# Kernel optimization log

Hardware: AMD Instinct MI355X
Metric: run time of the kernel (lower is better)

The kernel has to match this reference:

```python
import jax, jax.numpy as jnp
import numpy as np

B, NDET, NT, NY, NX = 4, 128, 2048, 256, 256
D, L, NH, PS = 256, 6, 8, 16
HP, WP = NY // PS, NX // PS
N = HP * WP


def setup_inputs() -> dict:
    key = jax.random.key(0)
    ks = jax.random.split(key, 12)
    w = lambda k, s: jax.random.normal(k, s, jnp.float32) * 0.02
    sino = jax.random.normal(ks[0], (B, 1, NDET, NT), jnp.float32)
    # LUT: channel 0 = floor temporal index (float, some out-of-range -> masked), channel 1 = interp alpha
    kf = jax.random.randint(ks[1], (NY, NX, NDET), -8, NT).astype(jnp.float32)
    alpha = jax.random.uniform(ks[2], (NY, NX, NDET), dtype=jnp.float32)
    lut = jnp.stack([kf, alpha], axis=-1)
    return {
        "sino": sino, "lut": lut,
        "patch_w": w(ks[3], (D, PS * PS)), "patch_b": jnp.zeros((D,), jnp.float32),
        "pos_embed": w(ks[4], (1, N, D)),
        "ln1_g": jnp.ones((L, D), jnp.float32), "ln1_b": jnp.zeros((L, D), jnp.float32),
        "wqkv": w(ks[5], (L, 3 * D, D)), "bqkv": jnp.zeros((L, 3 * D), jnp.float32),
        "wo": w(ks[6], (L, D, D)), "bo": jnp.zeros((L, D), jnp.float32),
        "ln2_g": jnp.ones((L, D), jnp.float32), "ln2_b": jnp.zeros((L, D), jnp.float32),
        "w1": w(ks[7], (L, 4 * D, D)), "b1": jnp.zeros((L, 4 * D), jnp.float32),
        "w2": w(ks[8], (L, D, 4 * D)), "b2": jnp.zeros((L, D), jnp.float32),
        "proj_w": w(ks[9], (PS * PS, D)), "proj_b": jnp.zeros((PS * PS,), jnp.float32),
        "conv_w": w(ks[10], (1, 1, 3, 3)), "conv_b": jnp.zeros((1,), jnp.float32),
    }


def _layernorm(x, g, b):
    m = x.mean(-1, keepdims=True)
    v = x.var(-1, keepdims=True)
    return (x - m) / jnp.sqrt(v + 1e-5) * g + b


def _mha(x, wqkv, bqkv, wo, bo):
    Bq, Nt, Dd = x.shape
    hd = Dd // NH
    qkv = x @ wqkv.T + bqkv                       # [B,N,3D]
    q, k, v = jnp.split(qkv, 3, axis=-1)
    sp = lambda t: t.reshape(Bq, Nt, NH, hd).transpose(0, 2, 1, 3)  # [B,H,N,hd]
    q, k, v = sp(q), sp(k), sp(v)
    scores = jnp.einsum('bhnd,bhmd->bhnm', q, k) / jnp.sqrt(jnp.float32(hd))
    att = jax.nn.softmax(scores, axis=-1)
    o = jnp.einsum('bhnm,bhmd->bhnd', att, v).transpose(0, 2, 1, 3).reshape(Bq, Nt, Dd)
    return o @ wo.T + bo


def _backproject(sino, lut):
    # sino: [B,1,n_det,n_t]; lut: [ny,nx,n_det,2] -> image [B,1,ny,nx]
    n_t = sino.shape[-1]
    kf = lut[..., 0].astype(jnp.int32)
    alpha = lut[..., 1]
    valid = (kf >= 0) & (kf < n_t - 1)
    k0 = jnp.clip(kf, 0, n_t - 2)
    k1 = k0 + 1
    S = sino[:, 0]                                # [B, n_det, n_t]
    d_idx = jnp.arange(NDET)[None, None, :]       # broadcast over (ny, nx)

    def per_batch(Sb):                            # Sb: [n_det, n_t]
        s0 = Sb[d_idx, k0]                        # [ny,nx,n_det]
        s1 = Sb[d_idx, k1]
        sk = (1.0 - alpha) * s0 + alpha * s1
        return jnp.where(valid, sk, 0.0)

    sk = jax.vmap(per_batch)(S)                   # [B,ny,nx,n_det]
    apod = 0.5 - 0.5 * jnp.cos(2.0 * jnp.pi * jnp.arange(NDET) / (NDET - 1))
    apod = apod.astype(sino.dtype)
    out = jnp.einsum('byxd,d->byx', sk, apod) / jnp.maximum(apod.sum(), 1e-6)
    return out[:, None]                           # [B,1,ny,nx]


def reference(sino, lut, patch_w, patch_b, pos_embed, ln1_g, ln1_b, wqkv, bqkv,
              wo, bo, ln2_g, ln2_b, w1, b1, w2, b2, proj_w, proj_b, conv_w, conv_b):
    bp_img = _backproject(sino, lut)              # [B,1,NY,NX]
    # patch embed (Conv2d k=stride=patch  ==  patch-flatten + linear)
    x = bp_img[:, 0].reshape(B, HP, PS, WP, PS).transpose(0, 1, 3, 2, 4).reshape(B, N, PS * PS)
    z = x @ patch_w.T + patch_b                   # [B,N,D]
    z = z + pos_embed
    for l in range(L):
        y = _layernorm(z, ln1_g[l], ln1_b[l])
        z = z + _mha(y, wqkv[l], bqkv[l], wo[l], bo[l])
        y = _layernorm(z, ln2_g[l], ln2_b[l])
        y = jax.nn.gelu(y @ w1[l].T + b1[l], approximate=False) @ w2[l].T + b2[l]
        z = z + y
    pixels = z @ proj_w.T + proj_b                # [B,N,PS*PS]
    pixels = pixels.reshape(B, HP, WP, PS, PS).transpose(0, 1, 3, 2, 4)
    img = pixels.reshape(B, 1, HP * PS, WP * PS)
    img = jax.lax.conv_general_dilated(img, conv_w, (1, 1), 'SAME',
                                       dimension_numbers=('NCHW', 'OIHW', 'NCHW'))
    img = img + conv_b.reshape(1, 1, 1, 1)
    img = img + bp_img                            # residual (shapes match)
    return (img, bp_img)
```

## Files before the change

kernel.cpp:

```cpp
#include <hip/hip_runtime.h>
#include <hip/hip_bf16.h>
#include <math.h>

#define BB 4
#define NDET 128
#define NT 2048
#define DD 256
#define LL 6
#define MROWS 1024

typedef __attribute__((ext_vector_type(8))) short s8v;
typedef __attribute__((ext_vector_type(4))) float f32x4;
typedef unsigned short ushort_t;

__device__ __forceinline__ unsigned short f2b(float x) {
  union { float f; unsigned u; } v; v.f = x;
  unsigned r = v.u + 0x7fff + ((v.u >> 16) & 1);
  return (unsigned short)(r >> 16);
}
__device__ __forceinline__ unsigned pk2(float a, float b) {
  return (unsigned)f2b(a) | ((unsigned)f2b(b) << 16);
}
__device__ __forceinline__ float gelu_exact(float x) {
  return 0.5f * x * (1.0f + erff(x * 0.70710678118654752f));
}

__global__ __launch_bounds__(256) void cast_all(
    const float* __restrict__ s0, const float* __restrict__ s1,
    const float* __restrict__ s2, const float* __restrict__ s3,
    const float* __restrict__ s4, const float* __restrict__ s5,
    unsigned short* __restrict__ d0, unsigned short* __restrict__ d1,
    unsigned short* __restrict__ d2, unsigned short* __restrict__ d3,
    unsigned short* __restrict__ d4, unsigned short* __restrict__ d5,
    const float* __restrict__ sino, float* __restrict__ st)
{
  const int e0 = 16384, e1 = 311296, e2 = 409600, e3 = 802816, e4 = 1196032,
            e5 = 1212416, e6 = 1474560;
  int i = blockIdx.x * 256 + threadIdx.x;
  int stride = gridDim.x * 256;
  for (; i < e6; i += stride) {
    if (i < e5) {
      const float* s; unsigned short* d; int j;
      if (i < e0)      { s = s0; d = d0; j = i; }
      else if (i < e1) { s = s1; d = d1; j = i - e0; }
      else if (i < e2) { s = s2; d = d2; j = i - e1; }
      else if (i < e3) { s = s3; d = d3; j = i - e2; }
      else if (i < e4) { s = s4; d = d4; j = i - e3; }
      else             { s = s5; d = d5; j = i - e4; }
      float4 f = ((const float4*)s)[j];
      uint2 uv;
      uv.x = pk2(f.x, f.y);
      uv.y = pk2(f.z, f.w);
      ((uint2*)d)[j] = uv;
    } else {
      int idx = i - e5;
      float4 v;
      v.x = sino[idx];
      v.y = sino[262144 + idx];
      v.z = sino[524288 + idx];
      v.w = sino[786432 + idx];
      ((float4*)st)[idx] = v;
    }
  }
}

__global__ __launch_bounds__(256) void bp_part(
    const float* __restrict__ st, const float* __restrict__ lut,
    float* __restrict__ partial)
{
  __shared__ float apod[NDET];
  int tid = threadIdx.x;
  if (tid < NDET) {
    float ap = 0.5f - 0.5f * cosf(6.283185307179586f * (float)tid / 127.0f);
    apod[tid] = ap * (1.0f / 63.5f);
  }
  __syncthreads();
  int c = blockIdx.x & 7;
  int pb = blockIdx.x >> 3;
  int pix = pb * 256 + tid;
  const float* lrow = lut + (size_t)pix * 256;
  const float4* sp = (const float4*)st;
  float a0 = 0.f, a1 = 0.f, a2 = 0.f, a3 = 0.f;
#pragma unroll
  for (int d0 = c * 16; d0 < c * 16 + 16; d0 += 4) {
    float4 l0 = *(const float4*)(lrow + d0 * 2);
    float4 l1 = *(const float4*)(lrow + d0 * 2 + 4);
    float kfs[4] = {l0.x, l0.z, l1.x, l1.z};
    float als[4] = {l0.y, l0.w, l1.y, l1.w};
#pragma unroll
    for (int dd = 0; dd < 4; ++dd) {
      int kf = (int)kfs[dd];
      if (kf >= 0 && kf < NT - 1) {
        float al = als[dd];
        float ap = apod[d0 + dd];
        float w0 = (1.0f - al) * ap, w1 = al * ap;
        const float4* q = sp + (d0 + dd) * NT + kf;
        float4 s0 = q[0], s1 = q[1];
        a0 += w0 * s0.x + w1 * s1.x;
        a1 += w0 * s0.y + w1 * s1.y;
        a2 += w0 * s0.z + w1 * s1.z;
        a3 += w0 * s0.w + w1 * s1.w;
      }
    }
  }
  partial[(size_t)(c * 4 + 0) * 65536 + pix] = a0;
  partial[(size_t)(c * 4 + 1) * 65536 + pix] = a1;
  partial[(size_t)(c * 4 + 2) * 65536 + pix] = a2;
  partial[(size_t)(c * 4 + 3) * 65536 + pix] = a3;
}

__global__ __launch_bounds__(256) void bp_reduce(
    const float* __restrict__ partial, float* __restrict__ bp,
    float* __restrict__ out_bp)
{
  int pix = blockIdx.x * 256 + threadIdx.x;
#pragma unroll
  for (int b = 0; b < 4; ++b) {
    float s = 0.f;
#pragma unroll
    for (int c = 0; c < 8; ++c) s += partial[(size_t)(c * 4 + b) * 65536 + pix];
    bp[b * 65536 + pix] = s;
    out_bp[b * 65536 + pix] = s;
  }
}

template<int ACT, int RES, int AMODE, int OMODE, int TN>
__global__ __launch_bounds__(256) void gemm4(
    const float* __restrict__ A, const unsigned short* __restrict__ A16,
    const unsigned short* __restrict__ Wb,
    const float* __restrict__ bias, const float* __restrict__ res,
    const float* __restrict__ lng, const float* __restrict__ lnb,
    float* __restrict__ C, unsigned short* __restrict__ C16,
    int N, int K, int res_mask)
{
  constexpr int NJ = TN / 32;
  __shared__ __align__(16) unsigned short As[32][264];
  __shared__ __align__(16) unsigned short Bs[TN][264];
  int bm = blockIdx.y * 32, bn = blockIdx.x * TN;
  int tid = threadIdx.x;
  int lane = tid & 63, w = tid >> 6;
  int lr = lane & 15, hi = lane >> 4;
  int lk = hi * 8, lg = hi * 4;
  int wr = (w & 1) * 16, wc = (w >> 1) * (TN / 2 == 32 ? 32 : 16);
  f32x4 acc[NJ];
#pragma unroll
  for (int j = 0; j < NJ; ++j) acc[j] = (f32x4){0.f, 0.f, 0.f, 0.f};

  for (int kc = 0; kc < K; kc += 256) {
    if (kc) __syncthreads();
    if (AMODE == 2) {
      float4 gl = ((const float4*)lng)[lane];
      float4 bl = ((const float4*)lnb)[lane];
#pragma unroll
      for (int rr = 0; rr < 8; ++rr) {
        int row = w * 8 + rr;
        float4 v = ((const float4*)(A + (size_t)(bm + row) * 256))[lane];
        float s = v.x + v.y + v.z + v.w;
#pragma unroll
        for (int off = 32; off; off >>= 1) s += __shfl_xor(s, off);
        float mean = s * (1.0f / 256.0f);
        float q = (v.x - mean) * (v.x - mean) + (v.y - mean) * (v.y - mean) +
                  (v.z - mean) * (v.z - mean) + (v.w - mean) * (v.w - mean);
#pragma unroll
        for (int off = 32; off; off >>= 1) q += __shfl_xor(q, off);
        float inv = 1.0f / sqrtf(q * (1.0f / 256.0f) + 1e-5f);
        float y0 = (v.x - mean) * inv * gl.x + bl.x;
        float y1 = (v.y - mean) * inv * gl.y + bl.y;
        float y2 = (v.z - mean) * inv * gl.z + bl.z;
        float y3 = (v.w - mean) * inv * gl.w + bl.w;
        uint2 u2; u2.x = pk2(y0, y1); u2.y = pk2(y2, y3);
        *(uint2*)&As[row][lane * 4] = u2;
      }
    } else if (AMODE == 3) {
      int r = tid >> 3, cb = (tid & 7) * 32;
      const unsigned short* ap = A16 + (size_t)(bm + r) * K + kc + cb;
#pragma unroll
      for (int q8 = 0; q8 < 4; ++q8)
        *(uint4*)&As[r][cb + q8 * 8] = *(const uint4*)(ap + q8 * 8);
    } else {
      int r = tid >> 3, cb = (tid & 7) * 32;
#pragma unroll
      for (int q8 = 0; q8 < 4; ++q8) {
        int k = cb + q8 * 8;
        float4 f0, f1;
        if (AMODE == 0) {
          const float* ap = A + (size_t)(bm + r) * K + kc + k;
          f0 = *(const float4*)ap;
          f1 = *(const float4*)(ap + 4);
        } else {
          int m = bm + r;
          int bb = m >> 8, nn = m & 255;
          int k2 = k + 4;
          f0 = *(const float4*)(A + (size_t)bb * 65536 +
               ((nn >> 4) * 16 + (k >> 4)) * 256 + (nn & 15) * 16 + (k & 15));
          f1 = *(const float4*)(A + (size_t)bb * 65536 +
               ((nn >> 4) * 16 + (k2 >> 4)) * 256 + (nn & 15) * 16 + (k2 & 15));
        }
        uint4 u;
        u.x = pk2(f0.x, f0.y); u.y = pk2(f0.z, f0.w);
        u.z = pk2(f1.x, f1.y); u.w = pk2(f1.z, f1.w);
        *(uint4*)&As[r][k] = u;
      }
    }
    if (TN == 64) {
      int r = tid >> 2, cb = (tid & 3) * 64;
      const unsigned short* wp = Wb + (size_t)(bn + r) * K + kc + cb;
#pragma unroll
      for (int q8 = 0; q8 < 8; ++q8)
        *(uint4*)&Bs[r][cb + q8 * 8] = *(const uint4*)(wp + q8 * 8);
    } else {
      int r = tid >> 3, cb = (tid & 7) * 32;
      const unsigned short* wp = Wb + (size_t)(bn + r) * K + kc + cb;
#pragma unroll
      for (int q8 = 0; q8 < 4; ++q8)
        *(uint4*)&Bs[r][cb + q8 * 8] = *(const uint4*)(wp + q8 * 8);
    }
    __syncthreads();
#pragma unroll
    for (int k0 = 0; k0 < 256; k0 += 32) {
      s8v a = *(const s8v*)&As[wr + lr][k0 + lk];
      s8v b0 = *(const s8v*)&Bs[wc + lr][k0 + lk];
      acc[0] = __builtin_amdgcn_mfma_f32_16x16x32_bf16(a, b0, acc[0], 0, 0, 0);
      if (NJ == 2) {
        s8v b1 = *(const s8v*)&Bs[wc + 16 + lr][k0 + lk];
        acc[1] = __builtin_amdgcn_mfma_f32_16x16x32_bf16(a, b1, acc[1], 0, 0, 0);
      }
    }
  }

#pragma unroll
  for (int j = 0; j < NJ; ++j) {
    int n = bn + wc + j * 16 + lr;
    float bv = bias[n];
#pragma unroll
    for (int r4 = 0; r4 < 4; ++r4) {
      int m = bm + wr + lg + r4;
      float c = acc[j][r4] + bv;
      if (ACT == 1) c = gelu_exact(c);
      if (RES == 1) c += res[(size_t)(m & res_mask) * N + n];
      if (OMODE == 0) {
        C[(size_t)m * N + n] = c;
      } else if (OMODE == 1) {
        int bb = m >> 8, t2 = m & 255;
        C[(size_t)bb * 65536 + ((t2 >> 4) * 16 + (n >> 4)) * 256 +
          (t2 & 15) * 16 + (n & 15)] = c;
      } else {
        C16[(size_t)m * N + n] = f2b(c);
      }
    }
  }
}

__global__ __launch_bounds__(256) void attn_fused(
    const unsigned short* __restrict__ qkv, unsigned short* __restrict__ o16)
{
  __shared__ __align__(16) unsigned short Kl[256][40];
  __shared__ __align__(16) unsigned short Qb[32][40];
  __shared__ __align__(16) unsigned short Vt[32][264];
  __shared__ __align__(16) char sp[34304];
  float (*Sf)[268] = (float(*)[268])sp;
  unsigned short (*Pl)[264] = (unsigned short(*)[264])sp;
  int bi = blockIdx.x;
  int qc = bi & 7, h = (bi >> 3) & 7, b = bi >> 6;
  int tid = threadIdx.x, lane = tid & 63, w = tid >> 6;
  int lr = lane & 15, hi = lane >> 4;
  int lk = hi * 8, lg = hi * 4;
  const unsigned short* base = qkv + (size_t)b * 256 * 768;

  {
    const unsigned short* kr = base + tid * 768 + 256 + h * 32;
#pragma unroll
    for (int cq = 0; cq < 4; ++cq)
      *(uint4*)&Kl[tid][cq * 8] = *(const uint4*)(kr + cq * 8);
    const unsigned short* vr = base + tid * 768 + 512 + h * 32;
    unsigned short tmp[32];
#pragma unroll
    for (int cq = 0; cq < 4; ++cq)
      *(uint4*)&tmp[cq * 8] = *(const uint4*)(vr + cq * 8);
#pragma unroll
    for (int cc = 0; cc < 32; ++cc) Vt[cc][tid] = tmp[cc];
    int row = tid >> 3, c0 = (tid & 7) * 4;
    *(uint2*)&Qb[row][c0] =
        *(const uint2*)(base + (qc * 32 + row) * 768 + h * 32 + c0);
  }
  __syncthreads();

  {
    s8v qa0 = *(const s8v*)&Qb[lr][lk];
    s8v qa1 = *(const s8v*)&Qb[16 + lr][lk];
    f32x4 z4 = (f32x4){0.f, 0.f, 0.f, 0.f};
#pragma unroll
    for (int j = 0; j < 4; ++j) {
      s8v kb = *(const s8v*)&Kl[w * 64 + j * 16 + lr][lk];
      f32x4 s0 = __builtin_amdgcn_mfma_f32_16x16x32_bf16(qa0, kb, z4, 0, 0, 0);
      f32x4 s1 = __builtin_amdgcn_mfma_f32_16x16x32_bf16(qa1, kb, z4, 0, 0, 0);
#pragma unroll
      for (int r4 = 0; r4 < 4; ++r4) {
        Sf[lg + r4][w * 64 + j * 16 + lr] = s0[r4];
        Sf[16 + lg + r4][w * 64 + j * 16 + lr] = s1[r4];
      }
    }
  }
  __syncthreads();

  float vv[8][4];
  {
    const float scale = 0.17677669529663687f;
#pragma unroll
    for (int rr = 0; rr < 8; ++rr) {
      int row = w * 8 + rr;
      float4 v = *(const float4*)&Sf[row][lane * 4];
      v.x *= scale; v.y *= scale; v.z *= scale; v.w *= scale;
      float mx = fmaxf(fmaxf(v.x, v.y), fmaxf(v.z, v.w));
#pragma unroll
      for (int off = 32; off; off >>= 1) mx = fmaxf(mx, __shfl_xor(mx, off));
      float e0 = expf(v.x - mx), e1 = expf(v.y - mx);
      float e2 = expf(v.z - mx), e3 = expf(v.w - mx);
      float ss = e0 + e1 + e2 + e3;
#pragma unroll
      for (int off = 32; off; off >>= 1) ss += __shfl_xor(ss, off);
      float inv = 1.0f / ss;
      vv[rr][0] = e0 * inv; vv[rr][1] = e1 * inv;
      vv[rr][2] = e2 * inv; vv[rr][3] = e3 * inv;
    }
  }
  __syncthreads();
#pragma unroll
  for (int rr = 0; rr < 8; ++rr) {
    int row = w * 8 + rr;
    uint2 u2;
    u2.x = pk2(vv[rr][0], vv[rr][1]);
    u2.y = pk2(vv[rr][2], vv[rr][3]);
    *(uint2*)&Pl[row][lane * 4] = u2;
  }
  __syncthreads();

  {
    int wr = (w & 1) * 16, wc2 = (w >> 1) * 16;
    f32x4 oa = (f32x4){0.f, 0.f, 0.f, 0.f};
#pragma unroll
    for (int ks = 0; ks < 8; ++ks) {
      s8v pa = *(const s8v*)&Pl[wr + lr][ks * 32 + lk];
      s8v vb = *(const s8v*)&Vt[wc2 + lr][ks * 32 + lk];
      oa = __builtin_amdgcn_mfma_f32_16x16x32_bf16(pa, vb, oa, 0, 0, 0);
    }
#pragma unroll
    for (int r4 = 0; r4 < 4; ++r4) {
      int row = qc * 32 + wr + lg + r4;
      o16[((size_t)(b * 256) + row) * 256 + h * 32 + wc2 + lr] = f2b(oa[r4]);
    }
  }
}

__global__ __launch_bounds__(256) void conv_kernel(
    const float* __restrict__ img, const float* __restrict__ cw,
    const float* __restrict__ cb, const float* __restrict__ bp,
    float* __restrict__ out_img)
{
  int gid = blockIdx.x * 256 + threadIdx.x;
  int b = gid >> 16, rem = gid & 65535;
  int y = rem >> 8, x = rem & 255;
  const float* ip = img + (size_t)b * 65536;
  float s = cb[0];
#pragma unroll
  for (int dy = -1; dy <= 1; ++dy)
#pragma unroll
    for (int dx = -1; dx <= 1; ++dx) {
      int yy = y + dy, xx = x + dx;
      if (yy >= 0 && yy < 256 && xx >= 0 && xx < 256)
        s += cw[(dy + 1) * 3 + (dx + 1)] * ip[yy * 256 + xx];
    }
  out_img[gid] = s + bp[gid];
}

extern "C" void kernel_launch(void* const* d_in, const int* in_sizes, int n_in,
                              void* d_out, int out_size, void* d_ws, size_t ws_size,
                              hipStream_t stream) {
  const float* sino    = (const float*)d_in[0];
  const float* lut     = (const float*)d_in[1];
  const float* patch_w = (const float*)d_in[2];
  const float* patch_b = (const float*)d_in[3];
  const float* pos     = (const float*)d_in[4];
  const float* ln1_g   = (const float*)d_in[5];
  const float* ln1_b   = (const float*)d_in[6];
  const float* wqkv    = (const float*)d_in[7];
  const float* bqkv    = (const float*)d_in[8];
  const float* wo      = (const float*)d_in[9];
  const float* bo      = (const float*)d_in[10];
  const float* ln2_g   = (const float*)d_in[11];
  const float* ln2_b   = (const float*)d_in[12];
  const float* w1      = (const float*)d_in[13];
  const float* b1      = (const float*)d_in[14];
  const float* w2      = (const float*)d_in[15];
  const float* b2      = (const float*)d_in[16];
  const float* proj_w  = (const float*)d_in[17];
  const float* proj_b  = (const float*)d_in[18];
  const float* conv_w  = (const float*)d_in[19];
  const float* conv_b  = (const float*)d_in[20];
  float* out = (float*)d_out;
  float* ws  = (float*)d_ws;

  float* bpb     = ws;
  float* z       = bpb + 262144;
  float* imgp    = z + 262144;
  float* partial = imgp + 262144;
  float* st      = partial + 2097152;
  unsigned short* wsu    = (unsigned short*)(st + 1048576);
  unsigned short* pwb    = wsu;
  unsigned short* qkvw   = pwb + 65536;
  unsigned short* wow    = qkvw + 1179648;
  unsigned short* w1w    = wow + 393216;
  unsigned short* w2w    = w1w + 1572864;
  unsigned short* projw  = w2w + 1572864;
  unsigned short* qkvb16 = projw + 65536;
  unsigned short* hb16   = qkvb16 + 786432;
  unsigned short* ob16   = hb16 + 1048576;

  cast_all<<<2048, 256, 0, stream>>>(patch_w, wqkv, wo, w1, w2, proj_w,
                                     pwb, qkvw, wow, w1w, w2w, projw,
                                     sino, st);
  bp_part<<<2048, 256, 0, stream>>>(st, lut, partial);
  bp_reduce<<<256, 256, 0, stream>>>(partial, bpb, out + 262144);

  gemm4<0, 1, 1, 0, 32><<<dim3(8, 32), 256, 0, stream>>>(
      bpb, nullptr, pwb, patch_b, pos, nullptr, nullptr, z, nullptr,
      256, 256, 255);

  for (int l = 0; l < LL; ++l) {
    gemm4<0, 0, 2, 2, 64><<<dim3(12, 32), 256, 0, stream>>>(
        z, nullptr, qkvw + (size_t)l * 196608, bqkv + l * 768, nullptr,
        ln1_g + l * 256, ln1_b + l * 256, nullptr, qkvb16, 768, 256, 0);
    attn_fused<<<256, 256, 0, stream>>>(qkvb16, ob16);
    gemm4<0, 1, 3, 0, 32><<<dim3(8, 32), 256, 0, stream>>>(
        nullptr, ob16, wow + (size_t)l * 65536, bo + l * 256, z,
        nullptr, nullptr, z, nullptr, 256, 256, 1023);
    gemm4<1, 0, 2, 2, 64><<<dim3(16, 32), 256, 0, stream>>>(
        z, nullptr, w1w + (size_t)l * 262144, b1 + l * 1024, nullptr,
        ln2_g + l * 256, ln2_b + l * 256, nullptr, hb16, 1024, 256, 0);
    gemm4<0, 1, 3, 0, 32><<<dim3(8, 32), 256, 0, stream>>>(
        nullptr, hb16, w2w + (size_t)l * 262144, b2 + l * 256, z,
        nullptr, nullptr, z, nullptr, 256, 1024, 1023);
  }

  gemm4<0, 0, 0, 1, 32><<<dim3(8, 32), 256, 0, stream>>>(
      z, nullptr, projw, proj_b, nullptr, nullptr, nullptr, imgp, nullptr,
      256, 256, 0);
  conv_kernel<<<1024, 256, 0, stream>>>(imgp, conv_w, conv_b, bpb, out);
}
```

Baseline: 443.4 us.

## Fuse attention with output projection and batch backprojection sample loads

Attention and the Wo projection with bias and residual now run in one kernel. Each block owns 16 query rows of one batch, loops over all 8 heads, keeps the bf16 head outputs in shared memory, then multiplies them by Wo and adds the result into z. This removes a launch and the ob16 round trip through global memory, but the grid drops from 256 blocks to 64, K/V are reloaded per head per block, and there are many more barriers. Separately, the backprojection kernel clamps invalid indices to zero weight instead of branching and issues all 8 detector sample loads before accumulating, to expose more memory-level parallelism.

```diff
diff --git a/kernel.cpp b/kernel.cpp
--- a/kernel.cpp
+++ b/kernel.cpp
@@ -78,29 +78,38 @@
   int c = blockIdx.x & 7;
   int pb = blockIdx.x >> 3;
   int pix = pb * 256 + tid;
-  const float* lrow = lut + (size_t)pix * 256;
+  const float4* lrow4 = (const float4*)(lut + (size_t)pix * 256);
   const float4* sp = (const float4*)st;
   float a0 = 0.f, a1 = 0.f, a2 = 0.f, a3 = 0.f;
 #pragma unroll
-  for (int d0 = c * 16; d0 < c * 16 + 16; d0 += 4) {
-    float4 l0 = *(const float4*)(lrow + d0 * 2);
-    float4 l1 = *(const float4*)(lrow + d0 * 2 + 4);
-    float kfs[4] = {l0.x, l0.z, l1.x, l1.z};
-    float als[4] = {l0.y, l0.w, l1.y, l1.w};
-#pragma unroll
-    for (int dd = 0; dd < 4; ++dd) {
-      int kf = (int)kfs[dd];
-      if (kf >= 0 && kf < NT - 1) {
-        float al = als[dd];
-        float ap = apod[d0 + dd];
-        float w0 = (1.0f - al) * ap, w1 = al * ap;
-        const float4* q = sp + (d0 + dd) * NT + kf;
-        float4 s0 = q[0], s1 = q[1];
-        a0 += w0 * s0.x + w1 * s1.x;
-        a1 += w0 * s0.y + w1 * s1.y;
-        a2 += w0 * s0.z + w1 * s1.z;
-        a3 += w0 * s0.w + w1 * s1.w;
-      }
+  for (int half = 0; half < 2; ++half) {
+    int d0 = c * 16 + half * 8;
+    float4 l0 = lrow4[d0 / 2 + 0];
+    float4 l1 = lrow4[d0 / 2 + 1];
+    float4 l2 = lrow4[d0 / 2 + 2];
+    float4 l3 = lrow4[d0 / 2 + 3];
+    float kfa[8] = {l0.x, l0.z, l1.x, l1.z, l2.x, l2.z, l3.x, l3.z};
+    float ala[8] = {l0.y, l0.w, l1.y, l1.w, l2.y, l2.w, l3.y, l3.w};
+    float4 sv0[8], sv1[8];
+    float w0[8], w1[8];
+#pragma unroll
+    for (int dd = 0; dd < 8; ++dd) {
+      int kf = (int)kfa[dd];
+      bool valid = (kf >= 0) && (kf < NT - 1);
+      int kc = valid ? kf : 0;
+      float ap = valid ? apod[d0 + dd] : 0.f;
+      w0[dd] = (1.0f - ala[dd]) * ap;
+      w1[dd] = ala[dd] * ap;
+      const float4* q = sp + (d0 + dd) * NT + kc;
+      sv0[dd] = q[0];
+      sv1[dd] = q[1];
+    }
+#pragma unroll
+    for (int dd = 0; dd < 8; ++dd) {
+      a0 += w0[dd] * sv0[dd].x + w1[dd] * sv1[dd].x;
+      a1 += w0[dd] * sv0[dd].y + w1[dd] * sv1[dd].y;
+      a2 += w0[dd] * sv0[dd].z + w1[dd] * sv1[dd].z;
+      a3 += w0[dd] * sv0[dd].w + w1[dd] * sv1[dd].w;
     }
   }
   partial[(size_t)(c * 4 + 0) * 65536 + pix] = a0;
@@ -251,103 +260,135 @@
   }
 }
 
-__global__ __launch_bounds__(256) void attn_fused(
-    const unsigned short* __restrict__ qkv, unsigned short* __restrict__ o16)
-{
-  __shared__ __align__(16) unsigned short Kl[256][40];
-  __shared__ __align__(16) unsigned short Qb[32][40];
-  __shared__ __align__(16) unsigned short Vt[32][264];
-  __shared__ __align__(16) char sp[34304];
-  float (*Sf)[268] = (float(*)[268])sp;
-  unsigned short (*Pl)[264] = (unsigned short(*)[264])sp;
+__global__ __launch_bounds__(256) void attn_wo(
+    const unsigned short* __restrict__ qkv,
+    const unsigned short* __restrict__ wow, const float* __restrict__ bo,
+    float* __restrict__ z)
+{
+  __shared__ __align__(16) char smem[71424];
+  unsigned short (*Qb)[264] = (unsigned short(*)[264])(smem);
+  unsigned short (*Kl)[40]  = (unsigned short(*)[40])(smem + 8448);
+  unsigned short (*Vt)[264] = (unsigned short(*)[264])(smem + 28928);
+  float (*Sf)[268]          = (float(*)[268])(smem + 45824);
+  unsigned short (*Pl)[264] = (unsigned short(*)[264])(smem + 45824);
+  unsigned short (*Ob)[264] = (unsigned short(*)[264])(smem + 62976);
+  unsigned short (*Bs)[264] = (unsigned short(*)[264])(smem + 8448);
+
   int bi = blockIdx.x;
-  int qc = bi & 7, h = (bi >> 3) & 7, b = bi >> 6;
+  int rc = bi & 15, b = bi >> 4;
   int tid = threadIdx.x, lane = tid & 63, w = tid >> 6;
   int lr = lane & 15, hi = lane >> 4;
   int lk = hi * 8, lg = hi * 4;
+  int m0 = b * 256 + rc * 16;
   const unsigned short* base = qkv + (size_t)b * 256 * 768;
 
   {
-    const unsigned short* kr = base + tid * 768 + 256 + h * 32;
-#pragma unroll
-    for (int cq = 0; cq < 4; ++cq)
-      *(uint4*)&Kl[tid][cq * 8] = *(const uint4*)(kr + cq * 8);
-    const unsigned short* vr = base + tid * 768 + 512 + h * 32;
-    unsigned short tmp[32];
-#pragma unroll
-    for (int cq = 0; cq < 4; ++cq)
-      *(uint4*)&tmp[cq * 8] = *(const uint4*)(vr + cq * 8);
-#pragma unroll
-    for (int cc = 0; cc < 32; ++cc) Vt[cc][tid] = tmp[cc];
-    int row = tid >> 3, c0 = (tid & 7) * 4;
-    *(uint2*)&Qb[row][c0] =
-        *(const uint2*)(base + (qc * 32 + row) * 768 + h * 32 + c0);
+    int r = tid >> 4, c0 = (tid & 15) * 16;
+    const unsigned short* qp = base + (size_t)(rc * 16 + r) * 768 + c0;
+    *(uint4*)&Qb[r][c0] = *(const uint4*)qp;
+    *(uint4*)&Qb[r][c0 + 8] = *(const uint4*)(qp + 8);
+  }
+
+  for (int h = 0; h < 8; ++h) {
+    __syncthreads();
+    {
+      const unsigned short* kr = base + (size_t)tid * 768 + 256 + h * 32;
+      *(uint4*)&Kl[tid][0]  = *(const uint4*)kr;
+      *(uint4*)&Kl[tid][8]  = *(const uint4*)(kr + 8);
+      *(uint4*)&Kl[tid][16] = *(const uint4*)(kr + 16);
+      *(uint4*)&Kl[tid][24] = *(const uint4*)(kr + 24);
+      const unsigned short* vr = base + (size_t)tid * 768 + 512 + h * 32;
+      unsigned short tmp[32];
+      *(uint4*)&tmp[0]  = *(const uint4*)vr;
+      *(uint4*)&tmp[8]  = *(const uint4*)(vr + 8);
+      *(uint4*)&tmp[16] = *(const uint4*)(vr + 16);
+      *(uint4*)&tmp[24] = *(const uint4*)(vr + 24);
+#pragma unroll
+      for (int cc = 0; cc < 32; ++cc) Vt[cc][tid] = tmp[cc];
+    }
+    __syncthreads();
+    {
+      s8v qa = *(const s8v*)&Qb[lr][h * 32 + lk];
+      f32x4 z4 = (f32x4){0.f, 0.f, 0.f, 0.f};
+#pragma unroll
+      for (int j = 0; j < 4; ++j) {
+        s8v kb = *(const s8v*)&Kl[w * 64 + j * 16 + lr][lk];
+        f32x4 s0 = __builtin_amdgcn_mfma_f32_16x16x32_bf16(qa, kb, z4, 0, 0, 0);
+#pragma unroll
+        for (int r4 = 0; r4 < 4; ++r4)
+          Sf[lg + r4][w * 64 + j * 16 + lr] = s0[r4];
+      }
+    }
+    __syncthreads();
+    float vv[4][4];
+    {
+      const float scale = 0.17677669529663687f;
+#pragma unroll
+      for (int rr = 0; rr < 4; ++rr) {
+        int row = w * 4 + rr;
+        float4 v = *(const float4*)&Sf[row][lane * 4];
+        v.x *= scale; v.y *= scale; v.z *= scale; v.w *= scale;
+        float mx = fmaxf(fmaxf(v.x, v.y), fmaxf(v.z, v.w));
+#pragma unroll
+        for (int off = 32; off; off >>= 1) mx = fmaxf(mx, __shfl_xor(mx, off));
+        float e0 = expf(v.x - mx), e1 = expf(v.y - mx);
+        float e2 = expf(v.z - mx), e3 = expf(v.w - mx);
+        float ss = e0 + e1 + e2 + e3;
+#pragma unroll
+        for (int off = 32; off; off >>= 1) ss += __shfl_xor(ss, off);
+        float inv = 1.0f / ss;
+        vv[rr][0] = e0 * inv; vv[rr][1] = e1 * inv;
+        vv[rr][2] = e2 * inv; vv[rr][3] = e3 * inv;
+      }
+    }
+    __syncthreads();
+#pragma unroll
+    for (int rr = 0; rr < 4; ++rr) {
+      uint2 u2;
+      u2.x = pk2(vv[rr][0], vv[rr][1]);
+      u2.y = pk2(vv[rr][2], vv[rr][3]);
+      *(uint2*)&Pl[w * 4 + rr][lane * 4] = u2;
+    }
+    __syncthreads();
+    if (w < 2) {
+      f32x4 oa = (f32x4){0.f, 0.f, 0.f, 0.f};
+#pragma unroll
+      for (int ks = 0; ks < 8; ++ks) {
+        s8v pa = *(const s8v*)&Pl[lr][ks * 32 + lk];
+        s8v vb = *(const s8v*)&Vt[w * 16 + lr][ks * 32 + lk];
+        oa = __builtin_amdgcn_mfma_f32_16x16x32_bf16(pa, vb, oa, 0, 0, 0);
+      }
+#pragma unroll
+      for (int r4 = 0; r4 < 4; ++r4)
+        Ob[lg + r4][h * 32 + w * 16 + lr] = f2b(oa[r4]);
+    }
   }
   __syncthreads();
 
-  {
-    s8v qa0 = *(const s8v*)&Qb[lr][lk];
-    s8v qa1 = *(const s8v*)&Qb[16 + lr][lk];
-    f32x4 z4 = (f32x4){0.f, 0.f, 0.f, 0.f};
-#pragma unroll
-    for (int j = 0; j < 4; ++j) {
-      s8v kb = *(const s8v*)&Kl[w * 64 + j * 16 + lr][lk];
-      f32x4 s0 = __builtin_amdgcn_mfma_f32_16x16x32_bf16(qa0, kb, z4, 0, 0, 0);
-      f32x4 s1 = __builtin_amdgcn_mfma_f32_16x16x32_bf16(qa1, kb, z4, 0, 0, 0);
-#pragma unroll
-      for (int r4 = 0; r4 < 4; ++r4) {
-        Sf[lg + r4][w * 64 + j * 16 + lr] = s0[r4];
-        Sf[16 + lg + r4][w * 64 + j * 16 + lr] = s1[r4];
-      }
-    }
-  }
-  __syncthreads();
-
-  float vv[8][4];
-  {
-    const float scale = 0.17677669529663687f;
-#pragma unroll
-    for (int rr = 0; rr < 8; ++rr) {
-      int row = w * 8 + rr;
-      float4 v = *(const float4*)&Sf[row][lane * 4];
-      v.x *= scale; v.y *= scale; v.z *= scale; v.w *= scale;
-      float mx = fmaxf(fmaxf(v.x, v.y), fmaxf(v.z, v.w));
-#pragma unroll
-      for (int off = 32; off; off >>= 1) mx = fmaxf(mx, __shfl_xor(mx, off));
-      float e0 = expf(v.x - mx), e1 = expf(v.y - mx);
-      float e2 = expf(v.z - mx), e3 = expf(v.w - mx);
-      float ss = e0 + e1 + e2 + e3;
-#pragma unroll
-      for (int off = 32; off; off >>= 1) ss += __shfl_xor(ss, off);
-      float inv = 1.0f / ss;
-      vv[rr][0] = e0 * inv; vv[rr][1] = e1 * inv;
-      vv[rr][2] = e2 * inv; vv[rr][3] = e3 * inv;
-    }
-  }
-  __syncthreads();
-#pragma unroll
-  for (int rr = 0; rr < 8; ++rr) {
-    int row = w * 8 + rr;
-    uint2 u2;
-    u2.x = pk2(vv[rr][0], vv[rr][1]);
-    u2.y = pk2(vv[rr][2], vv[rr][3]);
-    *(uint2*)&Pl[row][lane * 4] = u2;
-  }
-  __syncthreads();
-
-  {
-    int wr = (w & 1) * 16, wc2 = (w >> 1) * 16;
-    f32x4 oa = (f32x4){0.f, 0.f, 0.f, 0.f};
-#pragma unroll
-    for (int ks = 0; ks < 8; ++ks) {
-      s8v pa = *(const s8v*)&Pl[wr + lr][ks * 32 + lk];
-      s8v vb = *(const s8v*)&Vt[wc2 + lr][ks * 32 + lk];
-      oa = __builtin_amdgcn_mfma_f32_16x16x32_bf16(pa, vb, oa, 0, 0, 0);
-    }
+  for (int nc = 0; nc < 4; ++nc) {
+    __syncthreads();
+    {
+      int r = tid >> 2, cb = (tid & 3) * 64;
+      const unsigned short* wp = wow + (size_t)(nc * 64 + r) * 256 + cb;
+#pragma unroll
+      for (int q8 = 0; q8 < 8; ++q8)
+        *(uint4*)&Bs[r][cb + q8 * 8] = *(const uint4*)(wp + q8 * 8);
+    }
+    __syncthreads();
+    f32x4 acc = (f32x4){0.f, 0.f, 0.f, 0.f};
+    int wc = w * 16;
+#pragma unroll
+    for (int k0 = 0; k0 < 256; k0 += 32) {
+      s8v a = *(const s8v*)&Ob[lr][k0 + lk];
+      s8v bb = *(const s8v*)&Bs[wc + lr][k0 + lk];
+      acc = __builtin_amdgcn_mfma_f32_16x16x32_bf16(a, bb, acc, 0, 0, 0);
+    }
+    int n = nc * 64 + wc + lr;
+    float bv = bo[n];
 #pragma unroll
     for (int r4 = 0; r4 < 4; ++r4) {
-      int row = qc * 32 + wr + lg + r4;
-      o16[((size_t)(b * 256) + row) * 256 + h * 32 + wc2 + lr] = f2b(oa[r4]);
+      int m = m0 + lg + r4;
+      z[(size_t)m * 256 + n] += acc[r4] + bv;
     }
   }
 }
@@ -414,7 +455,6 @@
   unsigned short* projw  = w2w + 1572864;
   unsigned short* qkvb16 = projw + 65536;
   unsigned short* hb16   = qkvb16 + 786432;
-  unsigned short* ob16   = hb16 + 1048576;
 
   cast_all<<<2048, 256, 0, stream>>>(patch_w, wqkv, wo, w1, w2, proj_w,
                                      pwb, qkvw, wow, w1w, w2w, projw,
@@ -430,10 +470,8 @@
     gemm4<0, 0, 2, 2, 64><<<dim3(12, 32), 256, 0, stream>>>(
         z, nullptr, qkvw + (size_t)l * 196608, bqkv + l * 768, nullptr,
         ln1_g + l * 256, ln1_b + l * 256, nullptr, qkvb16, 768, 256, 0);
-    attn_fused<<<256, 256, 0, stream>>>(qkvb16, ob16);
-    gemm4<0, 1, 3, 0, 32><<<dim3(8, 32), 256, 0, stream>>>(
-        nullptr, ob16, wow + (size_t)l * 65536, bo + l * 256, z,
-        nullptr, nullptr, z, nullptr, 256, 256, 1023);
+    attn_wo<<<64, 256, 0, stream>>>(qkvb16, wow + (size_t)l * 65536,
+                                    bo + l * 256, z);
     gemm4<1, 0, 2, 2, 64><<<dim3(16, 32), 256, 0, stream>>>(
         z, nullptr, w1w + (size_t)l * 262144, b1 + l * 1024, nullptr,
         ln2_g + l * 256, ln2_b + l * 256, nullptr, hb16, 1024, 256, 0);
```

Result: slower. 573.2 us (+29.3%).
